# Kernel optimization log

Measured on AMD Instinct MI355X. Metric: run time of the kernel, lower is better.

The kernel has to match this reference:

```python
import jax, jax.numpy as jnp
import numpy as np

B, T, C = 4, 4096, 512


def setup_inputs() -> dict:
    key = jax.random.key(0)
    ks = jax.random.split(key, 7)
    s = 1.0 / np.sqrt(C)  # ~ torch Linear init scale
    X = jax.random.normal(ks[0], (B, T, C), jnp.float32)
    S_n = jnp.zeros((B, C, C), jnp.float32)
    W_Q = jax.random.normal(ks[1], (C, C), jnp.float32) * s
    b_Q = jax.random.normal(ks[2], (C,), jnp.float32) * s
    W_K = jax.random.normal(ks[3], (C, C), jnp.float32) * s
    b_K = jax.random.normal(ks[4], (C,), jnp.float32) * s
    W_V = jax.random.normal(ks[5], (C, C), jnp.float32) * s
    b_V = jax.random.normal(ks[6], (C,), jnp.float32) * s
    return {"X": X, "S_n": S_n, "W_Q": W_Q, "b_Q": b_Q,
            "W_K": W_K, "b_K": b_K, "W_V": W_V, "b_V": b_V}


def reference(X, S_n, W_Q, b_Q, W_K, b_K, W_V, b_V):
    # forward_chunkwise with chunk_len = 1 (exact simplification):
    #   per step t (gamma g_t from linspace(0.96, 0.99, T)):
    #     inner_t = (q_t . k_t) * v_t            # D = gamma^0 = 1
    #     cross_t = (q_t @ S) * g_t              # e[:,0,:] = g^1
    #     O_t     = tanh(inner_t + cross_t)
    #     S      <- k_t^T v_t + g_t * S          # D[-1] = 1, g**chunk_len = g
    Bx, Tx, Cx = X.shape
    Q = X @ W_Q + b_Q  # [B,T,C]
    K = X @ W_K + b_K
    V = X @ W_V + b_V
    gammas = jnp.linspace(0.96, 0.99, Tx).astype(X.dtype)

    def step(S, inp):
        q, k, v, g = inp  # q,k,v: [B,C]; g: scalar
        inner = jnp.sum(q * k, axis=-1, keepdims=True) * v      # [B,C]
        cross = jnp.einsum('bc,bcd->bd', q, S) * g              # [B,C]
        O = jnp.tanh(inner + cross)
        S_new = jnp.einsum('bc,bd->bcd', k, v) + S * g          # [B,C,C]
        return S_new, O

    # original resets S_n to zeros regardless of the passed-in value
    S0 = jnp.zeros_like(S_n)
    S_final, O = jax.lax.scan(
        step, S0,
        (Q.transpose(1, 0, 2), K.transpose(1, 0, 2), V.transpose(1, 0, 2), gammas))
    out = O.transpose(1, 0, 2)  # [B,T,C]
    return out, S_final
```

## Files before the change

### kernel.cpp

```cpp
#include <hip/hip_runtime.h>
#include <math.h>

#define Bsz  4
#define Tlen 4096
#define Cdim 512
#define CUT  (-12.0f)
#define NBE  8388608

typedef unsigned int u32;
typedef _Float16 f16;
typedef __attribute__((ext_vector_type(8))) _Float16 f16x8;
typedef __attribute__((ext_vector_type(4))) float floatx4;
#define MFMA_F16(a,b,c) __builtin_amdgcn_mfma_f32_16x16x32_f16((a),(b),(c),0,0,0)

union pun8 { uint4 u; f16x8 f; };

__device__ __forceinline__ u32 pack2(f16 a, f16 b) {
    return (u32)__builtin_bit_cast(unsigned short, a) |
           ((u32)__builtin_bit_cast(unsigned short, b) << 16);
}
__device__ __forceinline__ u32 splitpack(float v) {
    f16 h = (f16)v;
    f16 l = (f16)(v - (float)h);
    return pack2(h, l);
}
__device__ __forceinline__ void unpack8(const u32* p, f16x8& h, f16x8& l) {
    uint4 q0 = *(const uint4*)p;
    uint4 q1 = *(const uint4*)(p + 4);
    pun8 ph, pl;
    ph.u.x = __builtin_amdgcn_perm(q0.y, q0.x, 0x05040100u);
    pl.u.x = __builtin_amdgcn_perm(q0.y, q0.x, 0x07060302u);
    ph.u.y = __builtin_amdgcn_perm(q0.w, q0.z, 0x05040100u);
    pl.u.y = __builtin_amdgcn_perm(q0.w, q0.z, 0x07060302u);
    ph.u.z = __builtin_amdgcn_perm(q1.y, q1.x, 0x05040100u);
    pl.u.z = __builtin_amdgcn_perm(q1.y, q1.x, 0x07060302u);
    ph.u.w = __builtin_amdgcn_perm(q1.w, q1.z, 0x05040100u);
    pl.u.w = __builtin_amdgcn_perm(q1.w, q1.z, 0x07060302u);
    h = ph.f; l = pl.f;
}
__device__ __forceinline__ float tanh_fast(float x) {
    return 1.0f - 2.0f / (__expf(2.0f * x) + 1.0f);
}

__global__ __launch_bounds__(256) void prep_kernel(
    const float* __restrict__ X,
    const float* __restrict__ WQ, const float* __restrict__ WK,
    const float* __restrict__ WV,
    f16* __restrict__ Xf, f16* __restrict__ WT,
    float* __restrict__ Lg, float* __restrict__ Wfin, int* __restrict__ sLo) {
    __shared__ char pshm[18432];
    int bid = blockIdx.x, tid = threadIdx.x;
    if (bid < 2048) {
        size_t i = ((size_t)bid * 256 + tid) * 16;
        float v[16];
#pragma unroll
        for (int j = 0; j < 4; ++j) {
            float4 a = *(const float4*)(X + i + j * 4);
            v[j*4+0]=a.x; v[j*4+1]=a.y; v[j*4+2]=a.z; v[j*4+3]=a.w;
        }
        uint4 o0, o1;
        o0.x = pack2((f16)v[0], (f16)v[1]);   o0.y = pack2((f16)v[2], (f16)v[3]);
        o0.z = pack2((f16)v[4], (f16)v[5]);   o0.w = pack2((f16)v[6], (f16)v[7]);
        o1.x = pack2((f16)v[8], (f16)v[9]);   o1.y = pack2((f16)v[10], (f16)v[11]);
        o1.z = pack2((f16)v[12], (f16)v[13]); o1.w = pack2((f16)v[14], (f16)v[15]);
        *(uint4*)(Xf + i) = o0;
        *(uint4*)(Xf + i + 8) = o1;
    } else if (bid < 2240) {
        f16* tile = (f16*)pshm;
        int wb = bid - 2048;
        int mat = wb >> 6, rem = wb & 63;
        int k0 = (rem >> 3) * 64, n0 = (rem & 7) * 64;
        const float* W = (mat == 0) ? WQ : (mat == 1) ? WK : WV;
        int row = tid >> 2, q = tid & 3;
        const float* src = W + (size_t)(k0 + row) * Cdim + n0 + q * 16;
        float vv[16];
#pragma unroll
        for (int j = 0; j < 4; ++j) {
            float4 v = *(const float4*)(src + j * 4);
            vv[j*4+0]=v.x; vv[j*4+1]=v.y; vv[j*4+2]=v.z; vv[j*4+3]=v.w;
        }
#pragma unroll
        for (int j = 0; j < 16; ++j) tile[(q * 16 + j) * 72 + row] = (f16)vv[j];
        __syncthreads();
        f16x8 r0 = *(const f16x8*)(tile + row * 72 + q * 16);
        f16x8 r1 = *(const f16x8*)(tile + row * 72 + q * 16 + 8);
        f16* dst = WT + ((size_t)mat * Cdim + n0 + row) * Cdim + k0 + q * 16;
        *(f16x8*)dst = r0;
        *(f16x8*)(dst + 8) = r1;
    } else {
        float* Lsh = (float*)pshm;
        float* sums = (float*)(pshm + 16400);
        float lg[16];
        float local = 0.f;
        int base = tid * 16;
#pragma unroll
        for (int i = 0; i < 16; ++i) {
            int t = base + i;
            float g = 0.96f + 0.03f * ((float)t * (1.0f / 4095.0f));
            lg[i] = logf(g);
            local += lg[i];
        }
        sums[tid] = local;
        __syncthreads();
        for (int off = 1; off < 256; off <<= 1) {
            float v = sums[tid];
            if (tid >= off) v += sums[tid - off];
            __syncthreads();
            sums[tid] = v;
            __syncthreads();
        }
        float pre = (tid == 0) ? 0.f : sums[tid - 1];
#pragma unroll
        for (int i = 0; i < 16; ++i) {
            Lsh[base + i] = pre;
            pre += lg[i];
        }
        if (tid == 255) Lsh[4096] = pre;
        __syncthreads();
        for (int t = tid; t < 4097; t += 256) Lg[t] = Lsh[t];
        float LT = Lsh[4096];
        for (int s = tid; s < 4096; s += 256) Wfin[s] = __expf(LT - Lsh[s + 1]);
        if (tid < 128) {
            float ref = Lsh[tid * 32 + 1];
            int st_hi = tid >> 2;
            int lo = st_hi;
            for (int st = 0; st < st_hi; ++st)
                if (ref - Lsh[st * 128 + 128] > CUT) { lo = st; break; }
            sLo[tid] = lo;
        }
    }
}

__global__ __launch_bounds__(256, 2) void qkv_mfma(
    const f16* __restrict__ Xf, const f16* __restrict__ WT,
    const float* __restrict__ bQ, const float* __restrict__ bK,
    const float* __restrict__ bV,
    f16* __restrict__ Qf, f16* __restrict__ Kf,
    f16* __restrict__ KT, f16* __restrict__ VT) {
    __shared__ char smem[34816];
    u32* sX = (u32*)smem;
    u32* sW = (u32*)(smem + 16384);
    f16* sB = (f16*)smem;

    int tid = threadIdx.x, lane = tid & 63, wid = tid >> 6;
    int l16 = lane & 15, quad = lane >> 4;
    int wm = wid & 1, wn = wid >> 1;
    int xb = blockIdx.x;
    int mat = xb >> 2, n0 = (xb & 3) * 128;
    int m0 = blockIdx.y * 128;

    floatx4 acc[4][4];
#pragma unroll
    for (int i = 0; i < 4; ++i)
#pragma unroll
        for (int j = 0; j < 4; ++j) acc[i][j] = (floatx4)0.f;

    int srow = tid >> 1, shalf = tid & 1;
    int arow_a = wm * 64 + l16, arow_b = wn * 64 + l16;
    int swz_f = (l16 & 7) << 2;

    for (int kc = 0; kc < Cdim; kc += 64) {
        __syncthreads();
        {
            const f16* gx = Xf + (size_t)(m0 + srow) * Cdim + kc + shalf * 32;
            const f16* gw = WT + ((size_t)(mat * Cdim) + n0 + srow) * Cdim + kc + shalf * 32;
            int wswz = (srow & 7) << 2;
#pragma unroll
            for (int k = 0; k < 4; ++k) {
                uint4 xv = *(const uint4*)(gx + k * 8);
                uint4 wv = *(const uint4*)(gw + k * 8);
                int w = shalf * 16 + k * 4;
                *(uint4*)&sX[srow * 32 + (w ^ wswz)] = xv;
                *(uint4*)&sW[srow * 32 + (w ^ wswz)] = wv;
            }
        }
        __syncthreads();
#pragma unroll
        for (int ks = 0; ks < 2; ++ks) {
            int w0 = ks * 16 + quad * 4;
            f16x8 af[4], bf[4];
#pragma unroll
            for (int mt = 0; mt < 4; ++mt)
                af[mt] = ((pun8*)&sX[(arow_a + mt * 16) * 32 + (w0 ^ swz_f)])->f;
#pragma unroll
            for (int nt = 0; nt < 4; ++nt)
                bf[nt] = ((pun8*)&sW[(arow_b + nt * 16) * 32 + (w0 ^ swz_f)])->f;
#pragma unroll
            for (int mt = 0; mt < 4; ++mt)
#pragma unroll
                for (int nt = 0; nt < 4; ++nt)
                    acc[mt][nt] = MFMA_F16(af[mt], bf[nt], acc[mt][nt]);
        }
    }

    const float* bias = (mat == 0) ? bQ : (mat == 1) ? bK : bV;
    float bv[4];
#pragma unroll
    for (int nt = 0; nt < 4; ++nt) bv[nt] = bias[n0 + wn * 64 + nt * 16 + l16];
    float cv[4][4][4];
#pragma unroll
    for (int mt = 0; mt < 4; ++mt)
#pragma unroll
        for (int nt = 0; nt < 4; ++nt)
#pragma unroll
            for (int r = 0; r < 4; ++r) cv[mt][nt][r] = acc[mt][nt][r] + bv[nt];

    int b = m0 >> 12, tloc = m0 & 4095;

    if (mat == 2) {
#pragma unroll
        for (int mt = 0; mt < 4; ++mt)
#pragma unroll
            for (int nt = 0; nt < 4; ++nt) {
                int d = n0 + wn * 64 + nt * 16 + l16;
                int t = tloc + wm * 64 + mt * 16 + quad * 4;
                uint2 w;
                w.x = pack2((f16)cv[mt][nt][0], (f16)cv[mt][nt][1]);
                w.y = pack2((f16)cv[mt][nt][2], (f16)cv[mt][nt][3]);
                *(uint2*)(VT + ((size_t)(b * Cdim + d)) * Tlen + t) = w;
            }
    } else {
        if (mat == 1) {
#pragma unroll
            for (int mt = 0; mt < 4; ++mt)
#pragma unroll
                for (int nt = 0; nt < 4; ++nt) {
                    int d = n0 + wn * 64 + nt * 16 + l16;
                    int t = tloc + wm * 64 + mt * 16 + quad * 4;
                    uint2 w;
                    w.x = pack2((f16)cv[mt][nt][0], (f16)cv[mt][nt][1]);
                    w.y = pack2((f16)cv[mt][nt][2], (f16)cv[mt][nt][3]);
                    *(uint2*)(KT + ((size_t)(b * Cdim + d)) * Tlen + t) = w;
                }
        }
        __syncthreads();
#pragma unroll
        for (int mt = 0; mt < 4; ++mt)
#pragma unroll
            for (int nt = 0; nt < 4; ++nt)
#pragma unroll
                for (int r = 0; r < 4; ++r)
                    sB[(wm * 64 + mt * 16 + quad * 4 + r) * 136 +
                       wn * 64 + nt * 16 + l16] = (f16)cv[mt][nt][r];
        __syncthreads();
        {
            f16* Out = (mat == 0) ? Qf : Kf;
            int r2 = tid >> 1, h2 = tid & 1;
            f16* dst = Out + (size_t)(m0 + r2) * Cdim + n0 + h2 * 64;
#pragma unroll
            for (int j = 0; j < 8; ++j)
                *(uint4*)(dst + j * 8) = *(const uint4*)(sB + r2 * 136 + h2 * 64 + j * 8);
        }
    }
}

__global__ __launch_bounds__(512, 4) void attn_mfma(
    const f16* __restrict__ Qf, const f16* __restrict__ Kf,
    const f16* __restrict__ VT, const float* __restrict__ Lg,
    const int* __restrict__ sLo, float* __restrict__ out) {
    __shared__ char smem[49664];
    u32* sQ  = (u32*)smem;
    u32* sPc = (u32*)(smem + 32768);

    int tid = threadIdx.x, lane = tid & 63, wid = tid >> 6;
    int l16 = lane & 15, quad = lane >> 4;

    int i = blockIdx.x;
    int halfsel = i >> 8, q = i & 255;
    int L = ((q & 7) << 5) | (q >> 3);
    int b = L >> 6, ttl = L & 63;
    int tt = halfsel ? (63 - ttl) : (64 + ttl);
    int t0 = tt * 32;
    size_t bT = (size_t)b * Tlen;
    int lo = sLo[tt], hi = tt >> 2;

    {
        int r = tid >> 4, c16 = tid & 15;
        const f16* src = Qf + (bT + t0 + r) * Cdim + c16 * 32;
        int wswz = (r & 7) << 2;
#pragma unroll
        for (int k = 0; k < 4; ++k) {
            uint4 v = *(const uint4*)(src + k * 8);
            int w = c16 * 16 + k * 4;
            *(uint4*)&sQ[r * 256 + (w ^ wswz)] = v;
        }
    }

    float aT[2][4];
#pragma unroll
    for (int mt = 0; mt < 2; ++mt)
#pragma unroll
        for (int r = 0; r < 4; ++r)
            aT[mt][r] = Lg[t0 + mt * 16 + quad * 4 + r + 1];

    floatx4 oacc[2][4];
#pragma unroll
    for (int mt = 0; mt < 2; ++mt)
#pragma unroll
        for (int nt = 0; nt < 4; ++nt) oacc[mt][nt] = (floatx4)0.f;

    int swz_f = (l16 & 7) << 2;
    int rowA0 = l16 * 256;
    int rowA1 = (16 + l16) * 256;

    __syncthreads();

    for (int st = lo; st <= hi; ++st) {
        int s0 = st * 128;
        float lsp = Lg[s0 + wid * 16 + l16 + 1];

        floatx4 pacc[2];
        pacc[0] = (floatx4)0.f; pacc[1] = (floatx4)0.f;

        const f16* kb = Kf + (bT + s0 + wid * 16 + l16) * Cdim;
#pragma unroll 4
        for (int kc = 0; kc < 16; ++kc) {
            int ko = kc * 32 + quad * 8;
            int w0 = kc * 16 + quad * 4;
            f16x8 a0 = ((pun8*)&sQ[rowA0 + (w0 ^ swz_f)])->f;
            f16x8 a1 = ((pun8*)&sQ[rowA1 + (w0 ^ swz_f)])->f;
            f16x8 bk = *(const f16x8*)(kb + ko);
            pacc[0] = MFMA_F16(a0, bk, pacc[0]);
            pacc[1] = MFMA_F16(a1, bk, pacc[1]);
        }

        __syncthreads();
#pragma unroll
        for (int mt = 0; mt < 2; ++mt)
#pragma unroll
            for (int r = 0; r < 4; ++r) {
                int tl = mt * 16 + quad * 4 + r;
                int sl = wid * 16 + l16;
                int t = t0 + tl, s = s0 + sl;
                float p = pacc[mt][r];
                p = (s <= t) ? p * __expf(aT[mt][r] - lsp) : 0.f;
                sPc[tl * 132 + (sl ^ ((tl & 7) << 4))] = splitpack(p);
            }
        __syncthreads();

        const f16* vb = VT + ((size_t)(b * Cdim + wid * 64 + l16)) * Tlen + s0;
#pragma unroll
        for (int kf = 0; kf < 4; ++kf) {
            int sb = kf * 32 + quad * 8;
            f16x8 ph[2], pl[2];
#pragma unroll
            for (int mt = 0; mt < 2; ++mt) {
                int tl = mt * 16 + l16;
                unpack8(&sPc[tl * 132 + (sb ^ ((tl & 7) << 4))], ph[mt], pl[mt]);
            }
#pragma unroll
            for (int nt = 0; nt < 4; ++nt) {
                f16x8 vf = *(const f16x8*)(vb + (size_t)nt * 16 * Tlen + sb);
#pragma unroll
                for (int mt = 0; mt < 2; ++mt) {
                    oacc[mt][nt] = MFMA_F16(ph[mt], vf, oacc[mt][nt]);
                    oacc[mt][nt] = MFMA_F16(pl[mt], vf, oacc[mt][nt]);
                }
            }
        }
    }

#pragma unroll
    for (int mt = 0; mt < 2; ++mt)
#pragma unroll
        for (int nt = 0; nt < 4; ++nt)
#pragma unroll
            for (int r = 0; r < 4; ++r) {
                int t = t0 + mt * 16 + quad * 4 + r;
                int d = wid * 64 + nt * 16 + l16;
                out[(bT + t) * (size_t)Cdim + d] = tanh_fast(oacc[mt][nt][r]);
            }
}

__global__ __launch_bounds__(256) void sfinal_mfma(
    const f16* __restrict__ KT, const f16* __restrict__ VT,
    const float* __restrict__ Lg, const float* __restrict__ Wfin,
    float* __restrict__ S) {
    __shared__ f16 sA[64 * 72];
    __shared__ f16 sB2[64 * 72];
    int tid = threadIdx.x, lane = tid & 63, wid = tid >> 6;
    int l16 = lane & 15, quad = lane >> 4;
    int wv_c = wid & 1, wv_d = wid >> 1;
    int c0 = blockIdx.x * 64, d0 = blockIdx.y * 64, b = blockIdx.z;
    float LT = Lg[Tlen];
    floatx4 acc[2][2];
#pragma unroll
    for (int i = 0; i < 2; ++i)
#pragma unroll
        for (int jj = 0; jj < 2; ++jj) acc[i][jj] = (floatx4)0.f;

    int s0start = Tlen - 64;
    for (int s0 = 0; s0 < Tlen; s0 += 64)
        if (LT - Lg[s0 + 64] > CUT) { s0start = s0; break; }

    int row = tid >> 2, q = tid & 3;
    for (int s0 = s0start; s0 < Tlen; s0 += 64) {
        __syncthreads();
        {
            const f16* g = KT + ((size_t)(b * Cdim + c0 + row)) * Tlen + s0 + q * 16;
            f16x8 u0 = *(const f16x8*)g;
            f16x8 u1 = *(const f16x8*)(g + 8);
            float wv[16];
#pragma unroll
            for (int jj = 0; jj < 4; ++jj) {
                float4 w4 = *(const float4*)(Wfin + s0 + q * 16 + jj * 4);
                wv[jj*4+0]=w4.x; wv[jj*4+1]=w4.y; wv[jj*4+2]=w4.z; wv[jj*4+3]=w4.w;
            }
            f16x8 o0, o1;
#pragma unroll
            for (int jj = 0; jj < 8; ++jj) o0[jj] = (f16)((float)u0[jj] * wv[jj]);
#pragma unroll
            for (int jj = 0; jj < 8; ++jj) o1[jj] = (f16)((float)u1[jj] * wv[8 + jj]);
            *(f16x8*)(sA + row * 72 + q * 16) = o0;
            *(f16x8*)(sA + row * 72 + q * 16 + 8) = o1;
            const f16* gv = VT + ((size_t)(b * Cdim + d0 + row)) * Tlen + s0 + q * 16;
            uint4 v0 = *(const uint4*)gv, v1 = *(const uint4*)(gv + 8);
            *(uint4*)(sB2 + row * 72 + q * 16) = v0;
            *(uint4*)(sB2 + row * 72 + q * 16 + 8) = v1;
        }
        __syncthreads();
#pragma unroll
        for (int ks = 0; ks < 2; ++ks) {
            int ko = ks * 32 + quad * 8;
            f16x8 a0 = *(const f16x8*)(sA + (wv_c * 32 + l16) * 72 + ko);
            f16x8 a1 = *(const f16x8*)(sA + (wv_c * 32 + 16 + l16) * 72 + ko);
            f16x8 b0 = *(const f16x8*)(sB2 + (wv_d * 32 + l16) * 72 + ko);
            f16x8 b1 = *(const f16x8*)(sB2 + (wv_d * 32 + 16 + l16) * 72 + ko);
            acc[0][0] = MFMA_F16(a0, b0, acc[0][0]);
            acc[0][1] = MFMA_F16(a0, b1, acc[0][1]);
            acc[1][0] = MFMA_F16(a1, b0, acc[1][0]);
            acc[1][1] = MFMA_F16(a1, b1, acc[1][1]);
        }
    }
#pragma unroll
    for (int ct = 0; ct < 2; ++ct)
#pragma unroll
        for (int dt = 0; dt < 2; ++dt)
#pragma unroll
            for (int r = 0; r < 4; ++r) {
                int c = c0 + wv_c * 32 + ct * 16 + quad * 4 + r;
                int d = d0 + wv_d * 32 + dt * 16 + l16;
                S[((size_t)(b * Cdim + c)) * Cdim + d] = acc[ct][dt][r];
            }
}

extern "C" void kernel_launch(void* const* d_in, const int* in_sizes, int n_in,
                              void* d_out, int out_size, void* d_ws, size_t ws_size,
                              hipStream_t stream) {
    (void)in_sizes; (void)n_in; (void)out_size; (void)ws_size;
    const float* X  = (const float*)d_in[0];
    const float* WQ = (const float*)d_in[2];
    const float* bQ = (const float*)d_in[3];
    const float* WK = (const float*)d_in[4];
    const float* bK = (const float*)d_in[5];
    const float* WV = (const float*)d_in[6];
    const float* bV = (const float*)d_in[7];

    float* out   = (float*)d_out;
    float* S_out = out + (size_t)NBE;

    char* ws = (char*)d_ws;
    f16*   Xf   = (f16*)(ws);
    f16*   Qf   = (f16*)(ws + 2ull * NBE);
    f16*   Kf   = (f16*)(ws + 4ull * NBE);
    f16*   KT   = (f16*)(ws + 6ull * NBE);
    f16*   VT   = (f16*)(ws + 8ull * NBE);
    f16*   WT   = (f16*)(ws + 10ull * NBE);
    char*  tail = ws + 10ull * NBE + (2u << 20);
    float* Lg   = (float*)(tail);
    float* Wfin = (float*)(tail + 16512);
    int*   sLo  = (int*)(tail + 16512 + 16384);

    prep_kernel<<<2241, 256, 0, stream>>>(X, WQ, WK, WV, Xf, WT, Lg, Wfin, sLo);
    qkv_mfma<<<dim3(12, 128), 256, 0, stream>>>(Xf, WT, bQ, bK, bV, Qf, Kf, KT, VT);
    attn_mfma<<<512, 512, 0, stream>>>(Qf, Kf, VT, Lg, sLo, out);
    sfinal_mfma<<<dim3(8, 8, Bsz), 256, 0, stream>>>(KT, VT, Lg, Wfin, S_out);
}
```

Measured before the change: 260.0 us.

## Merge final-state kernel into attention launch and double-buffer P with V prefetch

Folds the separate S_final GEMM kernel into the attention kernel as 256 extra 512-thread blocks, removing one launch and letting that work run alongside the attention tiles. Inside the attention loop, the P tile is double-buffered in shared memory, which drops one barrier per step. V fragments are also prefetched into registers midway through the QK^T loop so their global latency overlaps the MFMAs. The cost is higher register pressure and more LDS per block (66.5 KB), which may lower occupancy under launch_bounds(512,4).

New measurement: 266.2 us. 2.4% more time.

```diff
diff --git a/kernel.cpp b/kernel.cpp
--- a/kernel.cpp
+++ b/kernel.cpp
@@ -256,14 +256,66 @@
 
 __global__ __launch_bounds__(512, 4) void attn_mfma(
     const f16* __restrict__ Qf, const f16* __restrict__ Kf,
-    const f16* __restrict__ VT, const float* __restrict__ Lg,
-    const int* __restrict__ sLo, float* __restrict__ out) {
-    __shared__ char smem[49664];
+    const f16* __restrict__ VT, const f16* __restrict__ KT,
+    const float* __restrict__ Lg, const float* __restrict__ Wfin,
+    const int* __restrict__ sLo, float* __restrict__ out,
+    float* __restrict__ S) {
+    __shared__ char smem[66560];
+    int tid = threadIdx.x, lane = tid & 63, wid = tid >> 6;
+    int l16 = lane & 15, quad = lane >> 4;
+
+    if (blockIdx.x >= 512) {
+        f16* sA  = (f16*)smem;
+        f16* sB2 = (f16*)(smem + 9216);
+        int r = blockIdx.x - 512;
+        int c0 = (r & 7) * 64, d0 = ((r >> 3) & 7) * 64, bb = r >> 6;
+        int wv_c = wid & 3, wv_d = wid >> 2;
+        float LT = Lg[Tlen];
+        floatx4 acc[2];
+        acc[0] = (floatx4)0.f; acc[1] = (floatx4)0.f;
+        int s0start = Tlen - 64;
+        for (int s0 = 0; s0 < Tlen; s0 += 64)
+            if (LT - Lg[s0 + 64] > CUT) { s0start = s0; break; }
+        int row = tid >> 3, q8 = (tid & 7) * 8;
+        for (int s0 = s0start; s0 < Tlen; s0 += 64) {
+            __syncthreads();
+            {
+                const f16* g = KT + ((size_t)(bb * Cdim + c0 + row)) * Tlen + s0 + q8;
+                f16x8 u0 = *(const f16x8*)g;
+                float4 w0 = *(const float4*)(Wfin + s0 + q8);
+                float4 w1 = *(const float4*)(Wfin + s0 + q8 + 4);
+                float wv[8] = {w0.x, w0.y, w0.z, w0.w, w1.x, w1.y, w1.z, w1.w};
+                f16x8 o0;
+#pragma unroll
+                for (int j = 0; j < 8; ++j) o0[j] = (f16)((float)u0[j] * wv[j]);
+                *(f16x8*)(sA + row * 72 + q8) = o0;
+                const f16* gv = VT + ((size_t)(bb * Cdim + d0 + row)) * Tlen + s0 + q8;
+                *(f16x8*)(sB2 + row * 72 + q8) = *(const f16x8*)gv;
+            }
+            __syncthreads();
+#pragma unroll
+            for (int ks = 0; ks < 2; ++ks) {
+                int ko = ks * 32 + quad * 8;
+                f16x8 a0 = *(const f16x8*)(sA + (wv_c * 16 + l16) * 72 + ko);
+                f16x8 b0 = *(const f16x8*)(sB2 + (wv_d * 32 + l16) * 72 + ko);
+                f16x8 b1 = *(const f16x8*)(sB2 + (wv_d * 32 + 16 + l16) * 72 + ko);
+                acc[0] = MFMA_F16(a0, b0, acc[0]);
+                acc[1] = MFMA_F16(a0, b1, acc[1]);
+            }
+        }
+#pragma unroll
+        for (int dt = 0; dt < 2; ++dt)
+#pragma unroll
+            for (int rr = 0; rr < 4; ++rr) {
+                int c = c0 + wv_c * 16 + quad * 4 + rr;
+                int d = d0 + wv_d * 32 + dt * 16 + l16;
+                S[((size_t)(bb * Cdim + c)) * Cdim + d] = acc[dt][rr];
+            }
+        return;
+    }
+
     u32* sQ  = (u32*)smem;
     u32* sPc = (u32*)(smem + 32768);
-
-    int tid = threadIdx.x, lane = tid & 63, wid = tid >> 6;
-    int l16 = lane & 15, quad = lane >> 4;
 
     int i = blockIdx.x;
     int halfsel = i >> 8, q = i & 255;
@@ -305,6 +357,7 @@
 
     __syncthreads();
 
+    int pb = 0;
     for (int st = lo; st <= hi; ++st) {
         int s0 = st * 128;
         float lsp = Lg[s0 + wid * 16 + l16 + 1];
@@ -313,8 +366,10 @@
         pacc[0] = (floatx4)0.f; pacc[1] = (floatx4)0.f;
 
         const f16* kb = Kf + (bT + s0 + wid * 16 + l16) * Cdim;
+        const f16* vb = VT + ((size_t)(b * Cdim + wid * 64 + l16)) * Tlen + s0;
+
 #pragma unroll 4
-        for (int kc = 0; kc < 16; ++kc) {
+        for (int kc = 0; kc < 8; ++kc) {
             int ko = kc * 32 + quad * 8;
             int w0 = kc * 16 + quad * 4;
             f16x8 a0 = ((pun8*)&sQ[rowA0 + (w0 ^ swz_f)])->f;
@@ -324,7 +379,26 @@
             pacc[1] = MFMA_F16(a1, bk, pacc[1]);
         }
 
-        __syncthreads();
+        f16x8 vpre[2][4];
+#pragma unroll
+        for (int kf = 0; kf < 2; ++kf)
+#pragma unroll
+            for (int nt = 0; nt < 4; ++nt)
+                vpre[kf][nt] = *(const f16x8*)(vb + (size_t)nt * 16 * Tlen +
+                                               kf * 32 + quad * 8);
+
+#pragma unroll 4
+        for (int kc = 8; kc < 16; ++kc) {
+            int ko = kc * 32 + quad * 8;
+            int w0 = kc * 16 + quad * 4;
+            f16x8 a0 = ((pun8*)&sQ[rowA0 + (w0 ^ swz_f)])->f;
+            f16x8 a1 = ((pun8*)&sQ[rowA1 + (w0 ^ swz_f)])->f;
+            f16x8 bk = *(const f16x8*)(kb + ko);
+            pacc[0] = MFMA_F16(a0, bk, pacc[0]);
+            pacc[1] = MFMA_F16(a1, bk, pacc[1]);
+        }
+
+        u32* sP = sPc + pb * 4224;
 #pragma unroll
         for (int mt = 0; mt < 2; ++mt)
 #pragma unroll
@@ -334,11 +408,18 @@
                 int t = t0 + tl, s = s0 + sl;
                 float p = pacc[mt][r];
                 p = (s <= t) ? p * __expf(aT[mt][r] - lsp) : 0.f;
-                sPc[tl * 132 + (sl ^ ((tl & 7) << 4))] = splitpack(p);
-            }
-        __syncthreads();
-
-        const f16* vb = VT + ((size_t)(b * Cdim + wid * 64 + l16)) * Tlen + s0;
+                sP[tl * 132 + (sl ^ ((tl & 7) << 4))] = splitpack(p);
+            }
+        __syncthreads();
+
+        f16x8 vrest[2][4];
+#pragma unroll
+        for (int kf = 0; kf < 2; ++kf)
+#pragma unroll
+            for (int nt = 0; nt < 4; ++nt)
+                vrest[kf][nt] = *(const f16x8*)(vb + (size_t)nt * 16 * Tlen +
+                                                (kf + 2) * 32 + quad * 8);
+
 #pragma unroll
         for (int kf = 0; kf < 4; ++kf) {
             int sb = kf * 32 + quad * 8;
@@ -346,11 +427,11 @@
 #pragma unroll
             for (int mt = 0; mt < 2; ++mt) {
                 int tl = mt * 16 + l16;
-                unpack8(&sPc[tl * 132 + (sb ^ ((tl & 7) << 4))], ph[mt], pl[mt]);
+                unpack8(&sP[tl * 132 + (sb ^ ((tl & 7) << 4))], ph[mt], pl[mt]);
             }
 #pragma unroll
             for (int nt = 0; nt < 4; ++nt) {
-                f16x8 vf = *(const f16x8*)(vb + (size_t)nt * 16 * Tlen + sb);
+                f16x8 vf = (kf < 2) ? vpre[kf][nt] : vrest[kf - 2][nt];
 #pragma unroll
                 for (int mt = 0; mt < 2; ++mt) {
                     oacc[mt][nt] = MFMA_F16(ph[mt], vf, oacc[mt][nt]);
@@ -358,6 +439,7 @@
                 }
             }
         }
+        pb ^= 1;
     }
 
 #pragma unroll
@@ -369,78 +451,6 @@
                 int t = t0 + mt * 16 + quad * 4 + r;
                 int d = wid * 64 + nt * 16 + l16;
                 out[(bT + t) * (size_t)Cdim + d] = tanh_fast(oacc[mt][nt][r]);
-            }
-}
-
-__global__ __launch_bounds__(256) void sfinal_mfma(
-    const f16* __restrict__ KT, const f16* __restrict__ VT,
-    const float* __restrict__ Lg, const float* __restrict__ Wfin,
-    float* __restrict__ S) {
-    __shared__ f16 sA[64 * 72];
-    __shared__ f16 sB2[64 * 72];
-    int tid = threadIdx.x, lane = tid & 63, wid = tid >> 6;
-    int l16 = lane & 15, quad = lane >> 4;
-    int wv_c = wid & 1, wv_d = wid >> 1;
-    int c0 = blockIdx.x * 64, d0 = blockIdx.y * 64, b = blockIdx.z;
-    float LT = Lg[Tlen];
-    floatx4 acc[2][2];
-#pragma unroll
-    for (int i = 0; i < 2; ++i)
-#pragma unroll
-        for (int jj = 0; jj < 2; ++jj) acc[i][jj] = (floatx4)0.f;
-
-    int s0start = Tlen - 64;
-    for (int s0 = 0; s0 < Tlen; s0 += 64)
-        if (LT - Lg[s0 + 64] > CUT) { s0start = s0; break; }
-
-    int row = tid >> 2, q = tid & 3;
-    for (int s0 = s0start; s0 < Tlen; s0 += 64) {
-        __syncthreads();
-        {
-            const f16* g = KT + ((size_t)(b * Cdim + c0 + row)) * Tlen + s0 + q * 16;
-            f16x8 u0 = *(const f16x8*)g;
-            f16x8 u1 = *(const f16x8*)(g + 8);
-            float wv[16];
-#pragma unroll
-            for (int jj = 0; jj < 4; ++jj) {
-                float4 w4 = *(const float4*)(Wfin + s0 + q * 16 + jj * 4);
-                wv[jj*4+0]=w4.x; wv[jj*4+1]=w4.y; wv[jj*4+2]=w4.z; wv[jj*4+3]=w4.w;
-            }
-            f16x8 o0, o1;
-#pragma unroll
-            for (int jj = 0; jj < 8; ++jj) o0[jj] = (f16)((float)u0[jj] * wv[jj]);
-#pragma unroll
-            for (int jj = 0; jj < 8; ++jj) o1[jj] = (f16)((float)u1[jj] * wv[8 + jj]);
-            *(f16x8*)(sA + row * 72 + q * 16) = o0;
-            *(f16x8*)(sA + row * 72 + q * 16 + 8) = o1;
-            const f16* gv = VT + ((size_t)(b * Cdim + d0 + row)) * Tlen + s0 + q * 16;
-            uint4 v0 = *(const uint4*)gv, v1 = *(const uint4*)(gv + 8);
-            *(uint4*)(sB2 + row * 72 + q * 16) = v0;
-            *(uint4*)(sB2 + row * 72 + q * 16 + 8) = v1;
-        }
-        __syncthreads();
-#pragma unroll
-        for (int ks = 0; ks < 2; ++ks) {
-            int ko = ks * 32 + quad * 8;
-            f16x8 a0 = *(const f16x8*)(sA + (wv_c * 32 + l16) * 72 + ko);
-            f16x8 a1 = *(const f16x8*)(sA + (wv_c * 32 + 16 + l16) * 72 + ko);
-            f16x8 b0 = *(const f16x8*)(sB2 + (wv_d * 32 + l16) * 72 + ko);
-            f16x8 b1 = *(const f16x8*)(sB2 + (wv_d * 32 + 16 + l16) * 72 + ko);
-            acc[0][0] = MFMA_F16(a0, b0, acc[0][0]);
-            acc[0][1] = MFMA_F16(a0, b1, acc[0][1]);
-            acc[1][0] = MFMA_F16(a1, b0, acc[1][0]);
-            acc[1][1] = MFMA_F16(a1, b1, acc[1][1]);
-        }
-    }
-#pragma unroll
-    for (int ct = 0; ct < 2; ++ct)
-#pragma unroll
-        for (int dt = 0; dt < 2; ++dt)
-#pragma unroll
-            for (int r = 0; r < 4; ++r) {
-                int c = c0 + wv_c * 32 + ct * 16 + quad * 4 + r;
-                int d = d0 + wv_d * 32 + dt * 16 + l16;
-                S[((size_t)(b * Cdim + c)) * Cdim + d] = acc[ct][dt][r];
             }
 }
 
@@ -473,6 +483,5 @@
 
     prep_kernel<<<2241, 256, 0, stream>>>(X, WQ, WK, WV, Xf, WT, Lg, Wfin, sLo);
     qkv_mfma<<<dim3(12, 128), 256, 0, stream>>>(Xf, WT, bQ, bK, bV, Qf, Kf, KT, VT);
-    attn_mfma<<<512, 512, 0, stream>>>(Qf, Kf, VT, Lg, sLo, out);
-    sfinal_mfma<<<dim3(8, 8, Bsz), 256, 0, stream>>>(KT, VT, Lg, Wfin, S_out);
-}
+    attn_mfma<<<768, 512, 0, stream>>>(Qf, Kf, VT, KT, Lg, Wfin, sLo, out, S_out);
+}
```

## Drop transposed K copy, stage V transpose through LDS, prefetch X tiles

Applied to the files above, without the earlier changes.

The QKV projection no longer writes a separate transposed K buffer. The final-state kernel now reads row-major K and transposes it while staging into shared memory, applying the per-step decay weight per row. The V transpose store is staged through LDS so global writes become coalesced rows, and X tiles are register-prefetched one k-step ahead. Together these remove a full f16 K write and reduce strided global stores. In exchange the sfinal kernel does scalar, bank-conflict-prone LDS transposes.

Result: slower. 292.0 us (+12.3%).

```diff
diff --git a/kernel.cpp b/kernel.cpp
--- a/kernel.cpp
+++ b/kernel.cpp
@@ -136,11 +136,12 @@
     const float* __restrict__ bQ, const float* __restrict__ bK,
     const float* __restrict__ bV,
     f16* __restrict__ Qf, f16* __restrict__ Kf,
-    f16* __restrict__ KT, f16* __restrict__ VT) {
+    f16* __restrict__ VT) {
     __shared__ char smem[34816];
     u32* sX = (u32*)smem;
     u32* sW = (u32*)(smem + 16384);
     f16* sB = (f16*)smem;
+    f16* T  = (f16*)smem;
 
     int tid = threadIdx.x, lane = tid & 63, wid = tid >> 6;
     int l16 = lane & 15, quad = lane >> 4;
@@ -158,20 +159,29 @@
     int srow = tid >> 1, shalf = tid & 1;
     int arow_a = wm * 64 + l16, arow_b = wn * 64 + l16;
     int swz_f = (l16 & 7) << 2;
+    int wswz = (srow & 7) << 2;
+
+    const f16* gx_base = Xf + (size_t)(m0 + srow) * Cdim + shalf * 32;
+    const f16* gw_base = WT + ((size_t)(mat * Cdim) + n0 + srow) * Cdim + shalf * 32;
+
+    uint4 px[4];
+#pragma unroll
+    for (int k = 0; k < 4; ++k) px[k] = *(const uint4*)(gx_base + k * 8);
 
     for (int kc = 0; kc < Cdim; kc += 64) {
         __syncthreads();
         {
-            const f16* gx = Xf + (size_t)(m0 + srow) * Cdim + kc + shalf * 32;
-            const f16* gw = WT + ((size_t)(mat * Cdim) + n0 + srow) * Cdim + kc + shalf * 32;
-            int wswz = (srow & 7) << 2;
 #pragma unroll
             for (int k = 0; k < 4; ++k) {
-                uint4 xv = *(const uint4*)(gx + k * 8);
-                uint4 wv = *(const uint4*)(gw + k * 8);
+                uint4 wv = *(const uint4*)(gw_base + kc + k * 8);
                 int w = shalf * 16 + k * 4;
-                *(uint4*)&sX[srow * 32 + (w ^ wswz)] = xv;
+                *(uint4*)&sX[srow * 32 + (w ^ wswz)] = px[k];
                 *(uint4*)&sW[srow * 32 + (w ^ wswz)] = wv;
+            }
+            if (kc + 64 < Cdim) {
+#pragma unroll
+                for (int k = 0; k < 4; ++k)
+                    px[k] = *(const uint4*)(gx_base + kc + 64 + k * 8);
             }
         }
         __syncthreads();
@@ -208,31 +218,24 @@
     int b = m0 >> 12, tloc = m0 & 4095;
 
     if (mat == 2) {
+        __syncthreads();
 #pragma unroll
         for (int mt = 0; mt < 4; ++mt)
 #pragma unroll
             for (int nt = 0; nt < 4; ++nt) {
-                int d = n0 + wn * 64 + nt * 16 + l16;
-                int t = tloc + wm * 64 + mt * 16 + quad * 4;
-                uint2 w;
-                w.x = pack2((f16)cv[mt][nt][0], (f16)cv[mt][nt][1]);
-                w.y = pack2((f16)cv[mt][nt][2], (f16)cv[mt][nt][3]);
-                *(uint2*)(VT + ((size_t)(b * Cdim + d)) * Tlen + t) = w;
-            }
+                int dl = wn * 64 + nt * 16 + l16;
+                int tl = wm * 64 + mt * 16 + quad * 4;
+                *(u32*)(T + dl * 134 + tl)     = pack2((f16)cv[mt][nt][0], (f16)cv[mt][nt][1]);
+                *(u32*)(T + dl * 134 + tl + 2) = pack2((f16)cv[mt][nt][2], (f16)cv[mt][nt][3]);
+            }
+        __syncthreads();
+#pragma unroll 8
+        for (int dd = 0; dd < 32; ++dd) {
+            int dl = wid * 32 + dd;
+            u32 v = *(const u32*)(T + dl * 134 + lane * 2);
+            *(u32*)(VT + ((size_t)(b * Cdim + n0 + dl)) * Tlen + tloc + lane * 2) = v;
+        }
     } else {
-        if (mat == 1) {
-#pragma unroll
-            for (int mt = 0; mt < 4; ++mt)
-#pragma unroll
-                for (int nt = 0; nt < 4; ++nt) {
-                    int d = n0 + wn * 64 + nt * 16 + l16;
-                    int t = tloc + wm * 64 + mt * 16 + quad * 4;
-                    uint2 w;
-                    w.x = pack2((f16)cv[mt][nt][0], (f16)cv[mt][nt][1]);
-                    w.y = pack2((f16)cv[mt][nt][2], (f16)cv[mt][nt][3]);
-                    *(uint2*)(KT + ((size_t)(b * Cdim + d)) * Tlen + t) = w;
-                }
-        }
         __syncthreads();
 #pragma unroll
         for (int mt = 0; mt < 4; ++mt)
@@ -373,7 +376,7 @@
 }
 
 __global__ __launch_bounds__(256) void sfinal_mfma(
-    const f16* __restrict__ KT, const f16* __restrict__ VT,
+    const f16* __restrict__ Kf, const f16* __restrict__ VT,
     const float* __restrict__ Lg, const float* __restrict__ Wfin,
     float* __restrict__ S) {
     __shared__ f16 sA[64 * 72];
@@ -381,7 +384,7 @@
     int tid = threadIdx.x, lane = tid & 63, wid = tid >> 6;
     int l16 = lane & 15, quad = lane >> 4;
     int wv_c = wid & 1, wv_d = wid >> 1;
-    int c0 = blockIdx.x * 64, d0 = blockIdx.y * 64, b = blockIdx.z;
+    int c0 = blockIdx.x * 64, d0 = blockIdx.y * 64, bb = blockIdx.z;
     float LT = Lg[Tlen];
     floatx4 acc[2][2];
 #pragma unroll
@@ -393,30 +396,23 @@
     for (int s0 = 0; s0 < Tlen; s0 += 64)
         if (LT - Lg[s0 + 64] > CUT) { s0start = s0; break; }
 
-    int row = tid >> 2, q = tid & 3;
+    int rowS = tid >> 2, q = tid & 3;
     for (int s0 = s0start; s0 < Tlen; s0 += 64) {
         __syncthreads();
         {
-            const f16* g = KT + ((size_t)(b * Cdim + c0 + row)) * Tlen + s0 + q * 16;
-            f16x8 u0 = *(const f16x8*)g;
-            f16x8 u1 = *(const f16x8*)(g + 8);
-            float wv[16];
-#pragma unroll
-            for (int jj = 0; jj < 4; ++jj) {
-                float4 w4 = *(const float4*)(Wfin + s0 + q * 16 + jj * 4);
-                wv[jj*4+0]=w4.x; wv[jj*4+1]=w4.y; wv[jj*4+2]=w4.z; wv[jj*4+3]=w4.w;
-            }
-            f16x8 o0, o1;
-#pragma unroll
-            for (int jj = 0; jj < 8; ++jj) o0[jj] = (f16)((float)u0[jj] * wv[jj]);
-#pragma unroll
-            for (int jj = 0; jj < 8; ++jj) o1[jj] = (f16)((float)u1[jj] * wv[8 + jj]);
-            *(f16x8*)(sA + row * 72 + q * 16) = o0;
-            *(f16x8*)(sA + row * 72 + q * 16 + 8) = o1;
-            const f16* gv = VT + ((size_t)(b * Cdim + d0 + row)) * Tlen + s0 + q * 16;
-            uint4 v0 = *(const uint4*)gv, v1 = *(const uint4*)(gv + 8);
-            *(uint4*)(sB2 + row * 72 + q * 16) = v0;
-            *(uint4*)(sB2 + row * 72 + q * 16 + 8) = v1;
+            const f16* gk = Kf + ((size_t)(bb * Tlen + s0 + rowS)) * Cdim + c0 + q * 16;
+            f16x8 k0 = *(const f16x8*)gk;
+            f16x8 k1 = *(const f16x8*)(gk + 8);
+            float w = Wfin[s0 + rowS];
+#pragma unroll
+            for (int j = 0; j < 8; ++j)
+                sA[(q * 16 + j) * 72 + rowS] = (f16)((float)k0[j] * w);
+#pragma unroll
+            for (int j = 0; j < 8; ++j)
+                sA[(q * 16 + 8 + j) * 72 + rowS] = (f16)((float)k1[j] * w);
+            const f16* gv = VT + ((size_t)(bb * Cdim + d0 + rowS)) * Tlen + s0 + q * 16;
+            *(uint4*)(sB2 + rowS * 72 + q * 16) = *(const uint4*)gv;
+            *(uint4*)(sB2 + rowS * 72 + q * 16 + 8) = *(const uint4*)(gv + 8);
         }
         __syncthreads();
 #pragma unroll
@@ -440,7 +436,7 @@
             for (int r = 0; r < 4; ++r) {
                 int c = c0 + wv_c * 32 + ct * 16 + quad * 4 + r;
                 int d = d0 + wv_d * 32 + dt * 16 + l16;
-                S[((size_t)(b * Cdim + c)) * Cdim + d] = acc[ct][dt][r];
+                S[((size_t)(bb * Cdim + c)) * Cdim + d] = acc[ct][dt][r];
             }
 }
 
@@ -463,16 +459,15 @@
     f16*   Xf   = (f16*)(ws);
     f16*   Qf   = (f16*)(ws + 2ull * NBE);
     f16*   Kf   = (f16*)(ws + 4ull * NBE);
-    f16*   KT   = (f16*)(ws + 6ull * NBE);
-    f16*   VT   = (f16*)(ws + 8ull * NBE);
-    f16*   WT   = (f16*)(ws + 10ull * NBE);
-    char*  tail = ws + 10ull * NBE + (2u << 20);
+    f16*   VT   = (f16*)(ws + 6ull * NBE);
+    f16*   WT   = (f16*)(ws + 8ull * NBE);
+    char*  tail = ws + 8ull * NBE + (2u << 20);
     float* Lg   = (float*)(tail);
     float* Wfin = (float*)(tail + 16512);
     int*   sLo  = (int*)(tail + 16512 + 16384);
 
     prep_kernel<<<2241, 256, 0, stream>>>(X, WQ, WK, WV, Xf, WT, Lg, Wfin, sLo);
-    qkv_mfma<<<dim3(12, 128), 256, 0, stream>>>(Xf, WT, bQ, bK, bV, Qf, Kf, KT, VT);
+    qkv_mfma<<<dim3(12, 128), 256, 0, stream>>>(Xf, WT, bQ, bK, bV, Qf, Kf, VT);
     attn_mfma<<<512, 512, 0, stream>>>(Qf, Kf, VT, Lg, sLo, out);
-    sfinal_mfma<<<dim3(8, 8, Bsz), 256, 0, stream>>>(KT, VT, Lg, Wfin, S_out);
-}
+    sfinal_mfma<<<dim3(8, 8, Bsz), 256, 0, stream>>>(Kf, VT, Lg, Wfin, S_out);
+}
```
